# Kernel optimization log

Measured on AMD Instinct MI355X. Metric: run time of the kernel, lower is better.

Reference implementation:

```python
import jax, jax.numpy as jnp
import numpy as np


def setup_inputs() -> dict:
    key = jax.random.key(0)
    k1, k2 = jax.random.split(key)
    bs, dim = 8192, 768
    nl_vec = jax.random.normal(k1, (bs, dim), dtype=jnp.float32)
    code_vec = jax.random.normal(k2, (bs, dim), dtype=jnp.float32)
    return {"nl_vec": nl_vec, "code_vec": code_vec}


def reference(nl_vec, code_vec):
    # scores[i, j] = <nl_vec[i], code_vec[j]>  (GEMM form of the broadcast mult-sum)
    scores = jnp.einsum("id,jd->ij", nl_vec, code_vec)  # [bs, bs]
    bs = scores.shape[0]
    # CrossEntropyLoss with labels = arange(bs): mean over rows of (logsumexp - diag)
    lse = jax.nn.logsumexp(scores, axis=-1)             # [bs]
    diag = jnp.einsum("id,id->i", nl_vec, code_vec)     # scores[i, i]
    loss = jnp.mean(lse - diag)
    return (loss, code_vec, nl_vec)
```

## Files before the change

### kernel.cpp

```cpp
#include <hip/hip_runtime.h>

#define BS     8192
#define DIM    768
#define NPART  16
#define BM     128
#define BN     128
#define BK     64
#define PCOLS  (BS / NPART)
#define NJT    (PCOLS / BN)
#define NKT    (DIM / BK)
#define NEL    ((size_t)BS * DIM)
#define NEL4   (NEL / 4)
#define CTILE  (2 * NEL4 - 1)

typedef __bf16 bfrag_t __attribute__((ext_vector_type(8)));
typedef float  facc_t  __attribute__((ext_vector_type(4)));

typedef const __attribute__((address_space(1))) void gv_t;
typedef __attribute__((address_space(3))) void lv_t;

__device__ __forceinline__ void gll16(const void* g, void* l) {
  __builtin_amdgcn_global_load_lds((gv_t*)g, (lv_t*)l, 16, 0, 0);
}

__device__ __forceinline__ unsigned short f2bf(float f) {
  union { float f; unsigned u; } v; v.f = f;
  unsigned u = v.u;
  return (unsigned short)((u + 0x7FFFu + ((u >> 16) & 1u)) >> 16);
}

__global__ void prep_kernel(const float* __restrict__ nl, const float* __restrict__ cd,
                            unsigned short* __restrict__ nlb, unsigned short* __restrict__ cdb,
                            float* __restrict__ dg) {
  const int lane = threadIdx.x & 63;
  const int wave = threadIdx.x >> 6;
  const int row  = blockIdx.x * 4 + wave;
  const size_t rbase = (size_t)row * DIM;
  const float4* ar = reinterpret_cast<const float4*>(nl + rbase);
  const float4* br = reinterpret_cast<const float4*>(cd + rbase);
  ushort4* ba = reinterpret_cast<ushort4*>(nlb + rbase);
  ushort4* bb = reinterpret_cast<ushort4*>(cdb + rbase);

  float s = 0.f;
#pragma unroll
  for (int i = 0; i < 3; ++i) {
    int idx = lane + 64 * i;
    float4 x = ar[idx];
    float4 y = br[idx];
    ushort4 xb, yb;
    xb.x = f2bf(x.x); xb.y = f2bf(x.y); xb.z = f2bf(x.z); xb.w = f2bf(x.w);
    yb.x = f2bf(y.x); yb.y = f2bf(y.y); yb.z = f2bf(y.z); yb.w = f2bf(y.w);
    ba[idx] = xb;
    bb[idx] = yb;
    s += x.x * y.x + x.y * y.y + x.z * y.z + x.w * y.w;
  }
#pragma unroll
  for (int off = 32; off; off >>= 1) s += __shfl_xor(s, off, 64);
  if (lane == 0) dg[row] = s;
}

__device__ __forceinline__ float4 cc4(const float4* cd4, const float4* nl4, size_t i) {
  return (i < NEL4) ? cd4[i] : nl4[i - NEL4];
}

__global__ __launch_bounds__(256, 4) void gemm_lse_kernel(
    const unsigned short* __restrict__ Abf,
    const unsigned short* __restrict__ Bbf,
    const float* __restrict__ cdf, const float* __restrict__ nlf,
    float* __restrict__ outp,
    float* __restrict__ pm, float* __restrict__ pl) {
  __shared__ __align__(16) unsigned short As[BM * BK];
  __shared__ __align__(16) unsigned short Bs[BN * BK];

  const int tid  = threadIdx.x;
  const int lane = tid & 63;
  const int wave = tid >> 6;
  const int wm   = wave >> 1;
  const int wn   = wave & 1;
  const int l15  = lane & 15;
  const int l4   = lane >> 4;
  const int sw   = l15 & 7;
  const int cp   = blockIdx.x;
  const int rb   = blockIdx.y;

  {
    const float4* cd4 = reinterpret_cast<const float4*>(cdf);
    const float4* nl4 = reinterpret_cast<const float4*>(nlf);
    const size_t gtid = ((size_t)blockIdx.y * gridDim.x + blockIdx.x) * blockDim.x + tid;
    const size_t nthr = (size_t)gridDim.x * gridDim.y * blockDim.x;
    for (size_t m = 1 + gtid; m <= CTILE; m += nthr) {
      float4 A = cc4(cd4, nl4, m - 1);
      float4 B = cc4(cd4, nl4, m);
      float4 d;
      d.x = A.w; d.y = B.x; d.z = B.y; d.w = B.z;
      *reinterpret_cast<float4*>(outp + 4 * m) = d;
    }
    if (gtid == 0) {
      outp[0] = 0.f;
      outp[1] = cdf[0]; outp[2] = cdf[1]; outp[3] = cdf[2];
      outp[2 * NEL] = nlf[NEL - 1];
    }
  }

  int srow[4], sc8g[4];
#pragma unroll
  for (int t = 0; t < 4; ++t) {
    int u   = wave * 256 + t * 64 + lane;
    srow[t] = u >> 3;
    sc8g[t] = (u & 7) ^ (srow[t] & 7);
  }

  float mrun[4][4], lrun[4][4];
#pragma unroll
  for (int i = 0; i < 4; ++i)
#pragma unroll
    for (int r = 0; r < 4; ++r) { mrun[i][r] = -1e30f; lrun[i][r] = 0.f; }

  for (int jt = 0; jt < NJT; ++jt) {
    facc_t acc[4][4];
#pragma unroll
    for (int mt = 0; mt < 4; ++mt)
#pragma unroll
      for (int nt = 0; nt < 4; ++nt) acc[mt][nt] = (facc_t){0.f, 0.f, 0.f, 0.f};

    for (int kt = 0; kt < NKT; ++kt) {
      __syncthreads();
#pragma unroll
      for (int t = 0; t < 4; ++t) {
        size_t ldso = (size_t)(wave * 256 + t * 64) * 8;
        gll16(Abf + (size_t)(rb * BM + srow[t]) * DIM + kt * BK + sc8g[t] * 8, As + ldso);
        gll16(Bbf + (size_t)(cp * PCOLS + jt * BN + srow[t]) * DIM + kt * BK + sc8g[t] * 8, Bs + ldso);
      }
      __syncthreads();

#pragma unroll
      for (int ks = 0; ks < 2; ++ks) {
        const int k8 = ks * 4 + l4;
        bfrag_t af[4], bfv[4];
#pragma unroll
        for (int mt = 0; mt < 4; ++mt) {
          int row = wm * 64 + mt * 16 + l15;
          af[mt] = *reinterpret_cast<const bfrag_t*>(&As[row * BK + (k8 ^ sw) * 8]);
        }
#pragma unroll
        for (int nt = 0; nt < 4; ++nt) {
          int row = wn * 64 + nt * 16 + l15;
          bfv[nt] = *reinterpret_cast<const bfrag_t*>(&Bs[row * BK + (k8 ^ sw) * 8]);
        }
#pragma unroll
        for (int mt = 0; mt < 4; ++mt)
#pragma unroll
          for (int nt = 0; nt < 4; ++nt)
            acc[mt][nt] = __builtin_amdgcn_mfma_f32_16x16x32_bf16(af[mt], bfv[nt], acc[mt][nt], 0, 0, 0);
      }
    }

#pragma unroll
    for (int mt = 0; mt < 4; ++mt)
#pragma unroll
      for (int r = 0; r < 4; ++r) {
        float v0 = acc[mt][0][r], v1 = acc[mt][1][r], v2 = acc[mt][2][r], v3 = acc[mt][3][r];
        float tm = fmaxf(fmaxf(v0, v1), fmaxf(v2, v3));
        float mn = fmaxf(mrun[mt][r], tm);
        float sc = __expf(mrun[mt][r] - mn);
        lrun[mt][r] = lrun[mt][r] * sc +
                      __expf(v0 - mn) + __expf(v1 - mn) + __expf(v2 - mn) + __expf(v3 - mn);
        mrun[mt][r] = mn;
      }
  }

#pragma unroll
  for (int mask = 1; mask < 16; mask <<= 1)
#pragma unroll
    for (int mt = 0; mt < 4; ++mt)
#pragma unroll
      for (int r = 0; r < 4; ++r) {
        float om = __shfl_xor(mrun[mt][r], mask, 64);
        float ol = __shfl_xor(lrun[mt][r], mask, 64);
        float mn = fmaxf(mrun[mt][r], om);
        lrun[mt][r] = lrun[mt][r] * __expf(mrun[mt][r] - mn) + ol * __expf(om - mn);
        mrun[mt][r] = mn;
      }

  float* cm = reinterpret_cast<float*>(As);
  float* cl = reinterpret_cast<float*>(Bs);
  __syncthreads();
  if (l15 == 0) {
#pragma unroll
    for (int mt = 0; mt < 4; ++mt)
#pragma unroll
      for (int r = 0; r < 4; ++r) {
        int rl = wm * 64 + mt * 16 + l4 * 4 + r;
        cm[wn * BM + rl] = mrun[mt][r];
        cl[wn * BM + rl] = lrun[mt][r];
      }
  }
  __syncthreads();
  if (tid < BM) {
    float m0 = cm[tid], l0 = cl[tid];
    float m1 = cm[BM + tid], l1 = cl[BM + tid];
    float mn = fmaxf(m0, m1);
    float ll = l0 * __expf(m0 - mn) + l1 * __expf(m1 - mn);
    size_t g = (size_t)(rb * BM + tid) * NPART + cp;
    pm[g] = mn;
    pl[g] = ll;
  }
}

__global__ void loss_kernel(const float* __restrict__ pm, const float* __restrict__ pl,
                            const float* __restrict__ dg, float* __restrict__ out) {
  __shared__ float red[4];
  const int tid = threadIdx.x;
  const int r   = blockIdx.x * 256 + tid;

  const float4* pmr = reinterpret_cast<const float4*>(pm + (size_t)r * NPART);
  const float4* plr = reinterpret_cast<const float4*>(pl + (size_t)r * NPART);

  float m = -1e30f, l = 0.f;
#pragma unroll
  for (int q = 0; q < NPART / 4; ++q) {
    float4 mv = pmr[q];
    float4 lv = plr[q];
#pragma unroll
    for (int k = 0; k < 4; ++k) {
      float m2 = (&mv.x)[k], l2 = (&lv.x)[k];
      float mn = fmaxf(m, m2);
      l = l * __expf(m - mn) + l2 * __expf(m2 - mn);
      m = mn;
    }
  }
  float local = m + __logf(l) - dg[r];

#pragma unroll
  for (int off = 32; off; off >>= 1) local += __shfl_xor(local, off, 64);
  if ((tid & 63) == 0) red[tid >> 6] = local;
  __syncthreads();
  if (tid == 0) {
    float s = red[0] + red[1] + red[2] + red[3];
    atomicAdd(out, s / (float)BS);
  }
}

extern "C" void kernel_launch(void* const* d_in, const int* in_sizes, int n_in,
                              void* d_out, int out_size, void* d_ws, size_t ws_size,
                              hipStream_t stream) {
  const float* nl = (const float*)d_in[0];
  const float* cd = (const float*)d_in[1];
  float* out = (float*)d_out;

  unsigned short* nlb = (unsigned short*)d_ws;
  unsigned short* cdb = nlb + NEL;
  float* pm = (float*)(cdb + NEL);
  float* pl = pm + (size_t)BS * NPART;
  float* dg = pl + (size_t)BS * NPART;

  prep_kernel<<<BS / 4, 256, 0, stream>>>(nl, cd, nlb, cdb, dg);
  gemm_lse_kernel<<<dim3(NPART, BS / BM), 256, 0, stream>>>(nlb, cdb, cd, nl, out, pm, pl);
  loss_kernel<<<BS / 256, 256, 0, stream>>>(pm, pl, dg, out);
}
```

Baseline: 226.7 us.

## Switch score GEMM from bf16 to fp8 scaled MFMA with 128-deep K tiles

Inputs are converted to packed fp8 instead of bf16 in the prep kernel. The GEMM uses the 16x16x128 f8f6f4 scaled MFMA with unit scales, K tiles are widened to 128 bytes and the LDS fragment loads are rewritten to match. This halves operand bytes and doubles MFMA throughput per instruction. The cost is lower precision in the logsumexp scores, though the diagonal term stays in fp32.

```diff
diff --git a/kernel.cpp b/kernel.cpp
--- a/kernel.cpp
+++ b/kernel.cpp
@@ -5,16 +5,17 @@
 #define NPART  16
 #define BM     128
 #define BN     128
-#define BK     64
+#define BKB    128
 #define PCOLS  (BS / NPART)
 #define NJT    (PCOLS / BN)
-#define NKT    (DIM / BK)
+#define NKT    (DIM / BKB)
 #define NEL    ((size_t)BS * DIM)
 #define NEL4   (NEL / 4)
 #define CTILE  (2 * NEL4 - 1)
-
-typedef __bf16 bfrag_t __attribute__((ext_vector_type(8)));
-typedef float  facc_t  __attribute__((ext_vector_type(4)));
+#define SCL1   0x7F7F7F7F
+
+typedef float facc_t __attribute__((ext_vector_type(4)));
+typedef int   iv8    __attribute__((ext_vector_type(8)));
 
 typedef const __attribute__((address_space(1))) void gv_t;
 typedef __attribute__((address_space(3))) void lv_t;
@@ -23,14 +24,14 @@
   __builtin_amdgcn_global_load_lds((gv_t*)g, (lv_t*)l, 16, 0, 0);
 }
 
-__device__ __forceinline__ unsigned short f2bf(float f) {
-  union { float f; unsigned u; } v; v.f = f;
-  unsigned u = v.u;
-  return (unsigned short)((u + 0x7FFFu + ((u >> 16) & 1u)) >> 16);
+__device__ __forceinline__ int pk_fp8(float4 v) {
+  int w = __builtin_amdgcn_cvt_pk_fp8_f32(v.x, v.y, 0, false);
+  w = __builtin_amdgcn_cvt_pk_fp8_f32(v.z, v.w, w, true);
+  return w;
 }
 
 __global__ void prep_kernel(const float* __restrict__ nl, const float* __restrict__ cd,
-                            unsigned short* __restrict__ nlb, unsigned short* __restrict__ cdb,
+                            unsigned char* __restrict__ nl8, unsigned char* __restrict__ cd8,
                             float* __restrict__ dg) {
   const int lane = threadIdx.x & 63;
   const int wave = threadIdx.x >> 6;
@@ -38,8 +39,8 @@
   const size_t rbase = (size_t)row * DIM;
   const float4* ar = reinterpret_cast<const float4*>(nl + rbase);
   const float4* br = reinterpret_cast<const float4*>(cd + rbase);
-  ushort4* ba = reinterpret_cast<ushort4*>(nlb + rbase);
-  ushort4* bb = reinterpret_cast<ushort4*>(cdb + rbase);
+  int* ba = reinterpret_cast<int*>(nl8 + rbase);
+  int* bb = reinterpret_cast<int*>(cd8 + rbase);
 
   float s = 0.f;
 #pragma unroll
@@ -47,11 +48,8 @@
     int idx = lane + 64 * i;
     float4 x = ar[idx];
     float4 y = br[idx];
-    ushort4 xb, yb;
-    xb.x = f2bf(x.x); xb.y = f2bf(x.y); xb.z = f2bf(x.z); xb.w = f2bf(x.w);
-    yb.x = f2bf(y.x); yb.y = f2bf(y.y); yb.z = f2bf(y.z); yb.w = f2bf(y.w);
-    ba[idx] = xb;
-    bb[idx] = yb;
+    ba[idx] = pk_fp8(x);
+    bb[idx] = pk_fp8(y);
     s += x.x * y.x + x.y * y.y + x.z * y.z + x.w * y.w;
   }
 #pragma unroll
@@ -64,13 +62,13 @@
 }
 
 __global__ __launch_bounds__(256, 4) void gemm_lse_kernel(
-    const unsigned short* __restrict__ Abf,
-    const unsigned short* __restrict__ Bbf,
+    const unsigned char* __restrict__ A8,
+    const unsigned char* __restrict__ B8,
     const float* __restrict__ cdf, const float* __restrict__ nlf,
     float* __restrict__ outp,
     float* __restrict__ pm, float* __restrict__ pl) {
-  __shared__ __align__(16) unsigned short As[BM * BK];
-  __shared__ __align__(16) unsigned short Bs[BN * BK];
+  __shared__ __align__(16) unsigned char As[BM * BKB];
+  __shared__ __align__(16) unsigned char Bs[BN * BKB];
 
   const int tid  = threadIdx.x;
   const int lane = tid & 63;
@@ -80,6 +78,7 @@
   const int l15  = lane & 15;
   const int l4   = lane >> 4;
   const int sw   = l15 & 7;
+  const int kb2  = l4 * 2;
   const int cp   = blockIdx.x;
   const int rb   = blockIdx.y;
 
@@ -127,31 +126,31 @@
       __syncthreads();
 #pragma unroll
       for (int t = 0; t < 4; ++t) {
-        size_t ldso = (size_t)(wave * 256 + t * 64) * 8;
-        gll16(Abf + (size_t)(rb * BM + srow[t]) * DIM + kt * BK + sc8g[t] * 8, As + ldso);
-        gll16(Bbf + (size_t)(cp * PCOLS + jt * BN + srow[t]) * DIM + kt * BK + sc8g[t] * 8, Bs + ldso);
+        int ub = (wave * 256 + t * 64) * 16;
+        gll16(A8 + (size_t)(rb * BM + srow[t]) * DIM + kt * BKB + sc8g[t] * 16, As + ub);
+        gll16(B8 + (size_t)(cp * PCOLS + jt * BN + srow[t]) * DIM + kt * BKB + sc8g[t] * 16, Bs + ub);
       }
       __syncthreads();
 
-#pragma unroll
-      for (int ks = 0; ks < 2; ++ks) {
-        const int k8 = ks * 4 + l4;
-        bfrag_t af[4], bfv[4];
-#pragma unroll
-        for (int mt = 0; mt < 4; ++mt) {
-          int row = wm * 64 + mt * 16 + l15;
-          af[mt] = *reinterpret_cast<const bfrag_t*>(&As[row * BK + (k8 ^ sw) * 8]);
-        }
-#pragma unroll
-        for (int nt = 0; nt < 4; ++nt) {
-          int row = wn * 64 + nt * 16 + l15;
-          bfv[nt] = *reinterpret_cast<const bfrag_t*>(&Bs[row * BK + (k8 ^ sw) * 8]);
-        }
-#pragma unroll
-        for (int mt = 0; mt < 4; ++mt)
-#pragma unroll
-          for (int nt = 0; nt < 4; ++nt)
-            acc[mt][nt] = __builtin_amdgcn_mfma_f32_16x16x32_bf16(af[mt], bfv[nt], acc[mt][nt], 0, 0, 0);
+      iv8 bfv[4];
+#pragma unroll
+      for (int nt = 0; nt < 4; ++nt) {
+        const unsigned char* base = &Bs[(wn * 64 + nt * 16 + l15) * BKB];
+        int4 lo = *reinterpret_cast<const int4*>(base + ((kb2    ) ^ sw) * 16);
+        int4 hi = *reinterpret_cast<const int4*>(base + ((kb2 + 1) ^ sw) * 16);
+        iv8 b; b[0]=lo.x; b[1]=lo.y; b[2]=lo.z; b[3]=lo.w; b[4]=hi.x; b[5]=hi.y; b[6]=hi.z; b[7]=hi.w;
+        bfv[nt] = b;
+      }
+#pragma unroll
+      for (int mt = 0; mt < 4; ++mt) {
+        const unsigned char* base = &As[(wm * 64 + mt * 16 + l15) * BKB];
+        int4 lo = *reinterpret_cast<const int4*>(base + ((kb2    ) ^ sw) * 16);
+        int4 hi = *reinterpret_cast<const int4*>(base + ((kb2 + 1) ^ sw) * 16);
+        iv8 av; av[0]=lo.x; av[1]=lo.y; av[2]=lo.z; av[3]=lo.w; av[4]=hi.x; av[5]=hi.y; av[6]=hi.z; av[7]=hi.w;
+#pragma unroll
+        for (int nt = 0; nt < 4; ++nt)
+          acc[mt][nt] = __builtin_amdgcn_mfma_scale_f32_16x16x128_f8f6f4(
+              av, bfv[nt], acc[mt][nt], 0, 0, 0, SCL1, 0, SCL1);
       }
     }
 
@@ -248,13 +247,13 @@
   const float* cd = (const float*)d_in[1];
   float* out = (float*)d_out;
 
-  unsigned short* nlb = (unsigned short*)d_ws;
-  unsigned short* cdb = nlb + NEL;
-  float* pm = (float*)(cdb + NEL);
+  unsigned char* nl8 = (unsigned char*)d_ws;
+  unsigned char* cd8 = nl8 + NEL;
+  float* pm = (float*)(cd8 + NEL);
   float* pl = pm + (size_t)BS * NPART;
   float* dg = pl + (size_t)BS * NPART;
 
-  prep_kernel<<<BS / 4, 256, 0, stream>>>(nl, cd, nlb, cdb, dg);
-  gemm_lse_kernel<<<dim3(NPART, BS / BM), 256, 0, stream>>>(nlb, cdb, cd, nl, out, pm, pl);
+  prep_kernel<<<BS / 4, 256, 0, stream>>>(nl, cd, nl8, cd8, dg);
+  gemm_lse_kernel<<<dim3(NPART, BS / BM), 256, 0, stream>>>(nl8, cd8, cd, nl, out, pm, pl);
   loss_kernel<<<BS / 256, 256, 0, stream>>>(pm, pl, dg, out);
 }
```

Result: slower. 261.9 us (+15.5%).
